# Kernel tuning notes

Measured on AMD Instinct MI355X. Metric: run time of the kernel, lower is better.

The kernel has to match this reference:

```python
import jax, jax.numpy as jnp
import numpy as np

B, T, K = 1024, 1024, 48
START, STOP = 46, 47
NEG = -10000.0


def setup_inputs() -> dict:
    key = jax.random.key(0)
    k1, k2 = jax.random.split(key)
    feats = jax.random.normal(k1, (B, T, K), dtype=jnp.float32)
    transitions = jax.random.normal(k2, (K, K), dtype=jnp.float32)
    # CRF constraints exactly as in __init__: no transition into START, none out of STOP
    transitions = transitions.at[START, :].set(NEG).at[:, STOP].set(NEG)
    return {"feats": feats, "transitions": transitions}


def _viterbi_one(feats, transitions):
    # feats: [T, K]; transitions[next_tag, prev_tag]: [K, K]
    init = jnp.full((K,), NEG, dtype=feats.dtype).at[START].set(0.0)

    def step(forward_var, feat):
        # scores[next, prev] = forward_var[prev] + transitions[next, prev]
        scores = forward_var[None, :] + transitions
        bptr = jnp.argmax(scores, axis=1)                 # [K] best prev per next
        new_fv = jnp.max(scores, axis=1) + feat           # [K]
        return new_fv, bptr

    forward_var, bptrs = jax.lax.scan(step, init, feats)  # bptrs: [T, K]
    terminal = forward_var + transitions[STOP]
    best = jnp.argmax(terminal)
    path_score = terminal[best]

    # backtrack: carry = tag at time t, emit it, move to bptrs[t][tag]
    def back(tag, bp):
        return bp[tag], tag

    _, best_path = jax.lax.scan(back, best, bptrs, reverse=True)  # [T] in time order
    return path_score, best_path


def reference(feats, transitions):
    # vmap the (faithful, per-sequence) Viterbi decode over the batch
    scores, paths = jax.vmap(_viterbi_one, in_axes=(0, None))(feats, transitions)
    return scores, paths
```

## Files before the change

### kernel.cpp

```cpp
#include <hip/hip_runtime.h>
#include <float.h>


#define BB 1024
#define TT 1024
#define KK 48
#define CC 16
#define LL 64
#define NEGV -10000.0f

__device__ __forceinline__ float rdlane(float v, int l) {
  return __int_as_float(__builtin_amdgcn_readlane(__float_as_int(v), l));
}
__device__ __forceinline__ float max3f(float a, float b, float c) {
  return fmaxf(fmaxf(a, b), c);
}


#define FSTEP(T_, FEAT_)                                                   \
  {                                                                        \
    float fvr[KK];                                                         \
    _Pragma("unroll") for (int j = 0; j < 12; ++j) {                       \
      float4 v4 = *(const float4*)(&fvbuf[4 * j]);                         \
      fvr[4 * j + 0] = v4.x; fvr[4 * j + 1] = v4.y;                        \
      fvr[4 * j + 2] = v4.z; fvr[4 * j + 3] = v4.w;                        \
    }                                                                      \
    float s_[KK];                                                          \
    _Pragma("unroll") for (int p = 0; p < KK; ++p) {                       \
      s_[p] = fvr[p] + tr[p];                                              \
    }                                                                      \
    float part[16];                                                        \
    _Pragma("unroll") for (int g = 0; g < 16; ++g) {                       \
      part[g] = max3f(s_[3 * g], s_[3 * g + 1], s_[3 * g + 2]);            \
    }                                                                      \
    float q0 = max3f(part[0], part[1], part[2]);                           \
    float q1 = max3f(part[3], part[4], part[5]);                           \
    float q2 = max3f(part[6], part[7], part[8]);                           \
    float q3 = max3f(part[9], part[10], part[11]);                         \
    float q4 = max3f(part[12], part[13], part[14]);                        \
    float m_ = fmaxf(max3f(q0, q1, q2), max3f(q3, q4, part[15]));          \
    mp[(size_t)(T_)*KK] = m_;                                              \
    fv = m_ + (FEAT_);                                                     \
    __builtin_amdgcn_wave_barrier();                                       \
    fvbuf[lane] = fv;                                                      \
    __builtin_amdgcn_wave_barrier();                                       \
  }

__global__ __launch_bounds__(64, 1) void viterbi_fused(
    const float* __restrict__ feats, const float* __restrict__ trans,
    float* __restrict__ scores, float* __restrict__ mx,
    float* __restrict__ path) {
  __shared__ __align__(16) float fvbuf[64];
  __shared__ float tl[KK * KK];
  const int lane = threadIdx.x;
  const int b = blockIdx.x;
  const int rl = (lane < KK) ? lane : (KK - 1);

  float tr[KK];
#pragma unroll
  for (int j = 0; j < 12; ++j) {
    float4 t4 = *(const float4*)(trans + rl * KK + 4 * j);
    tr[4 * j + 0] = t4.x; tr[4 * j + 1] = t4.y;
    tr[4 * j + 2] = t4.z; tr[4 * j + 3] = t4.w;
  }
#pragma unroll
  for (int j = 0; j < KK; ++j) asm volatile("" : "+v"(tr[j]));
  const float tstop = trans[(KK - 1) * KK + rl];
  for (int i = lane; i < KK * KK; i += 64) tl[i] = trans[i];

  const float* fp = feats + (size_t)b * TT * KK + rl;
  float* mp = mx + (size_t)b * TT * KK + rl;

  float fv = (lane == 46) ? 0.0f : NEGV;
  __syncthreads();
  fvbuf[lane] = fv;
  __builtin_amdgcn_wave_barrier();

  if (lane < KK) {
    float fA[8], fB[8];
#pragma unroll
    for (int k = 0; k < 8; ++k) fA[k] = fp[(size_t)k * KK];

    for (int t0 = 0; t0 < TT; t0 += 16) {
#pragma unroll
      for (int k = 0; k < 8; ++k)
        fB[k] = fp[(size_t)((t0 + 8 + k) & (TT - 1)) * KK];
#pragma unroll
      for (int u = 0; u < 8; ++u) FSTEP(t0 + u, fA[u]);
#pragma unroll
      for (int k = 0; k < 8; ++k)
        fA[k] = fp[(size_t)((t0 + 16 + k) & (TT - 1)) * KK];
#pragma unroll
      for (int u = 0; u < 8; ++u) FSTEP(t0 + 8 + u, fB[u]);
    }
  }

  float v = (lane < KK) ? (fv + tstop) : -FLT_MAX;
  int idx = lane;
#pragma unroll
  for (int off = 32; off >= 1; off >>= 1) {
    float ov = __shfl_xor(v, off);
    int oi = __shfl_xor(idx, off);
    bool take = (ov > v) || (ov == v && oi < idx);
    v = take ? ov : v;
    idx = take ? oi : idx;
  }
  if (lane == 0) scores[b] = v;
  int tag = idx;

  asm volatile("s_waitcnt vmcnt(0)" ::: "memory");

  float topA = mp[(size_t)(TT - 1) * KK];
  float MA[8], FE[8], MB[8], FB2[8];
#pragma unroll
  for (int u = 0; u < 8; ++u) {
    MA[u] = mp[(size_t)(TT - 2 - u) * KK];
    FE[u] = fp[(size_t)(TT - 2 - u) * KK];
  }

  int myv = 0;
  for (int jb = TT - 1; jb >= 15; jb -= 16) {
#pragma unroll
    for (int u = 0; u < 8; ++u) {
      int r = jb - 9 - u; int rc = r < 0 ? 0 : r;
      MB[u] = mp[(size_t)rc * KK];
      FB2[u] = fp[(size_t)rc * KK];
    }
#pragma unroll
    for (int u = 0; u < 8; ++u) {
      const int j = jb - u;
      if (lane == (j & 63)) myv = tag;
      if ((j & 63) == 0) path[(size_t)b * TT + j + lane] = (float)myv;
      float Tg = (u == 0) ? topA : MA[u - 1];
      float target = rdlane(Tg, tag);
      float s = (MA[u] + FE[u]) + tl[tag * KK + rl];
      unsigned long long bal = __ballot(s == target);
      tag = (int)__builtin_ctzll(bal);
    }
    float topB = MA[7];
#pragma unroll
    for (int u = 0; u < 8; ++u) {
      int r = jb - 17 - u; int rc = r < 0 ? 0 : r;
      MA[u] = mp[(size_t)rc * KK];
      FE[u] = fp[(size_t)rc * KK];
    }
#pragma unroll
    for (int u = 0; u < 8; ++u) {
      const int j = jb - 8 - u;
      if (lane == (j & 63)) myv = tag;
      if ((j & 63) == 0) path[(size_t)b * TT + j + lane] = (float)myv;
      float Tg = (u == 0) ? topB : MB[u - 1];
      float target = rdlane(Tg, tag);
      float s = (MB[u] + FB2[u]) + tl[tag * KK + rl];
      unsigned long long bal = __ballot(s == target);
      tag = (int)__builtin_ctzll(bal);
    }
    topA = MB[7];
  }
}


__global__ __launch_bounds__(64, 1) void viterbi_fwd_f(
    const float* __restrict__ feats, const float* __restrict__ trans,
    float* __restrict__ scores, unsigned char* __restrict__ bptr,
    int* __restrict__ bestArr) {
  __shared__ __align__(16) float fvbuf[64];
  const int lane = threadIdx.x;
  const int b = blockIdx.x;
  const int rl = (lane < KK) ? lane : (KK - 1);

  float tr[KK];
#pragma unroll
  for (int j = 0; j < 12; ++j) {
    float4 t4 = *(const float4*)(trans + rl * KK + 4 * j);
    tr[4 * j + 0] = t4.x; tr[4 * j + 1] = t4.y;
    tr[4 * j + 2] = t4.z; tr[4 * j + 3] = t4.w;
  }
  const float tstop = trans[(KK - 1) * KK + rl];

  if (lane < KK) fvbuf[lane] = (lane == 46) ? 0.0f : NEGV;
  __builtin_amdgcn_wave_barrier();

  const float* fp = feats + (size_t)b * TT * KK + rl;
  unsigned char* bp = bptr + (size_t)b * TT * KK + lane;

  float fbuf[4];
#pragma unroll
  for (int k = 0; k < 4; ++k) fbuf[k] = fp[(size_t)k * KK];

  float fv = NEGV;
  for (int t0 = 0; t0 < TT; t0 += 4) {
#pragma unroll
    for (int u = 0; u < 4; ++u) {
      const int t = t0 + u;
      float fvr[KK];
#pragma unroll
      for (int j = 0; j < 12; ++j) {
        float4 v4 = *(const float4*)(&fvbuf[4 * j]);
        fvr[4 * j + 0] = v4.x; fvr[4 * j + 1] = v4.y;
        fvr[4 * j + 2] = v4.z; fvr[4 * j + 3] = v4.w;
      }
      __builtin_amdgcn_wave_barrier();

      float bs0 = fvr[0] + tr[0], bs1 = fvr[12] + tr[12];
      float bs2 = fvr[24] + tr[24], bs3 = fvr[36] + tr[36];
      int bi0 = 0, bi1 = 12, bi2 = 24, bi3 = 36;
#pragma unroll
      for (int p = 1; p < 12; ++p) {
        float s0 = fvr[p] + tr[p];
        float s1 = fvr[12 + p] + tr[12 + p];
        float s2 = fvr[24 + p] + tr[24 + p];
        float s3 = fvr[36 + p] + tr[36 + p];
        if (s0 > bs0) { bs0 = s0; bi0 = p; }
        if (s1 > bs1) { bs1 = s1; bi1 = 12 + p; }
        if (s2 > bs2) { bs2 = s2; bi2 = 24 + p; }
        if (s3 > bs3) { bs3 = s3; bi3 = 36 + p; }
      }
      bool c1 = bs1 > bs0;
      float m01 = c1 ? bs1 : bs0; int i01 = c1 ? bi1 : bi0;
      bool c3 = bs3 > bs2;
      float m23 = c3 ? bs3 : bs2; int i23 = c3 ? bi3 : bi2;
      bool cf = m23 > m01;
      float m = cf ? m23 : m01; int bpi = cf ? i23 : i01;

      float nfv = m + fbuf[u];
      int tpre = t + 4; if (tpre >= TT) tpre = 0;
      fbuf[u] = fp[(size_t)tpre * KK];

      if (lane < KK) {
        bp[(size_t)t * KK] = (unsigned char)bpi;
        fvbuf[lane] = nfv;
        fv = nfv;
      }
      __builtin_amdgcn_wave_barrier();
    }
  }

  float v = (lane < KK) ? (fv + tstop) : -FLT_MAX;
  int idx = lane;
#pragma unroll
  for (int off = 32; off >= 1; off >>= 1) {
    float ov = __shfl_xor(v, off);
    int oi = __shfl_xor(idx, off);
    bool take = (ov > v) || (ov == v && oi < idx);
    v = take ? ov : v;
    idx = take ? oi : idx;
  }
  if (lane == 0) { scores[b] = v; bestArr[b] = idx; }
}

__global__ __launch_bounds__(256) void bwd_map(
    const unsigned char* __restrict__ bptr, unsigned char* __restrict__ cmap) {
  const int lane = threadIdx.x & 63;
  const int wg = blockIdx.x * 4 + (threadIdx.x >> 6);
  const int b = wg >> 4;
  const int c = wg & (CC - 1);
  const int rl = (lane < KK) ? lane : (KK - 1);
  const unsigned char* bp = bptr + ((size_t)b * TT + (size_t)c * LL) * KK + rl;

  int x = rl;
  const int CH = 16;
  int cur[CH], nxt[CH];
#pragma unroll
  for (int j = 0; j < CH; ++j) cur[j] = bp[(size_t)(LL - CH + j) * KK];
  for (int tb = LL - CH; tb >= 0; tb -= CH) {
    if (tb >= CH) {
#pragma unroll
      for (int j = 0; j < CH; ++j) nxt[j] = bp[(size_t)(tb - CH + j) * KK];
    }
#pragma unroll
    for (int j = CH - 1; j >= 0; --j) x = __shfl(cur[j], x);
    if (tb >= CH) {
#pragma unroll
      for (int j = 0; j < CH; ++j) cur[j] = nxt[j];
    }
  }
  if (lane < KK) cmap[(size_t)wg * KK + lane] = (unsigned char)x;
}

__global__ __launch_bounds__(256) void bwd_entry(
    const unsigned char* __restrict__ cmap, const int* __restrict__ bestArr,
    int* __restrict__ entry) {
  const int lane = threadIdx.x & 63;
  const int b = blockIdx.x * 4 + (threadIdx.x >> 6);
  const int rl = (lane < KK) ? lane : (KK - 1);

  int rows[CC];
#pragma unroll
  for (int c = 0; c < CC; ++c) rows[c] = cmap[((size_t)b * CC + c) * KK + rl];

  int tag = bestArr[b];
  int ev = 0;
#pragma unroll
  for (int c = CC - 1; c >= 0; --c) {
    if (lane == c) ev = tag;
    tag = __shfl(rows[c], tag);
  }
  if (lane < CC) entry[b * CC + lane] = ev;
}

__global__ __launch_bounds__(256) void bwd_emit(
    const unsigned char* __restrict__ bptr, const int* __restrict__ entry,
    float* __restrict__ path) {
  const int lane = threadIdx.x & 63;
  const int wg = blockIdx.x * 4 + (threadIdx.x >> 6);
  const int b = wg >> 4;
  const int c = wg & (CC - 1);
  const int rl = (lane < KK) ? lane : (KK - 1);
  const unsigned char* bp = bptr + ((size_t)b * TT + (size_t)c * LL) * KK + rl;

  int x = entry[b * CC + c];
  int myv = 0;
  const int CH = 16;
  int cur[CH], nxt[CH];
#pragma unroll
  for (int j = 0; j < CH; ++j) cur[j] = bp[(size_t)(LL - CH + j) * KK];
  for (int tb = LL - CH; tb >= 0; tb -= CH) {
    if (tb >= CH) {
#pragma unroll
      for (int j = 0; j < CH; ++j) nxt[j] = bp[(size_t)(tb - CH + j) * KK];
    }
#pragma unroll
    for (int j = CH - 1; j >= 0; --j) {
      if (lane == tb + j) myv = x;
      x = __shfl(cur[j], x);
    }
    if (tb >= CH) {
#pragma unroll
      for (int j = 0; j < CH; ++j) cur[j] = nxt[j];
    }
  }
  path[(size_t)b * TT + (size_t)c * LL + lane] = (float)myv;
}

extern "C" void kernel_launch(void* const* d_in, const int* in_sizes, int n_in,
                              void* d_out, int out_size, void* d_ws,
                              size_t ws_size, hipStream_t stream) {
  const float* feats = (const float*)d_in[0];
  const float* trans = (const float*)d_in[1];
  float* out = (float*)d_out;

  const size_t MX_BYTES = (size_t)BB * TT * KK * sizeof(float);
  if (ws_size >= MX_BYTES) {
    float* mx = (float*)d_ws;
    viterbi_fused<<<dim3(BB), dim3(64), 0, stream>>>(feats, trans, out, mx,
                                                     out + BB);
  } else {
    unsigned char* bptr = (unsigned char*)d_ws;
    char* p = (char*)d_ws + (size_t)BB * TT * KK;
    int* bestArr = (int*)p;
    p += BB * sizeof(int);
    unsigned char* cmap = (unsigned char*)p;
    p += (size_t)BB * CC * KK;
    int* entry = (int*)p;

    viterbi_fwd_f<<<dim3(BB), dim3(64), 0, stream>>>(feats, trans, out, bptr,
                                                     bestArr);
    bwd_map<<<dim3(BB * CC / 4), dim3(256), 0, stream>>>(bptr, cmap);
    bwd_entry<<<dim3(BB / 4), dim3(256), 0, stream>>>(cmap, bestArr, entry);
    bwd_emit<<<dim3(BB * CC / 4), dim3(256), 0, stream>>>(bptr, entry,
                                                          out + BB);
  }
}
```

Baseline: 481.9 us.

## Pack two sequences per block and interleave their backtracks in one wave

Each block now runs two waves, each doing the forward Viterbi pass for its own sequence. After a block barrier, the second wave exits and the first wave backtracks both sequences at once, interleaving their two dependent ballot/readlane chains. The aim is to hide the latency of the serial backtrack by giving each step two independent chains to overlap. In exchange, half the waves sit idle during the backtrack, the block is more coupled, and per-lane register use roughly doubles in that phase.

```diff
diff --git a/kernel.cpp b/kernel.cpp
--- a/kernel.cpp
+++ b/kernel.cpp
@@ -21,7 +21,7 @@
   {                                                                        \
     float fvr[KK];                                                         \
     _Pragma("unroll") for (int j = 0; j < 12; ++j) {                       \
-      float4 v4 = *(const float4*)(&fvbuf[4 * j]);                         \
+      float4 v4 = *(const float4*)(&fvb[4 * j]);                           \
       fvr[4 * j + 0] = v4.x; fvr[4 * j + 1] = v4.y;                        \
       fvr[4 * j + 2] = v4.z; fvr[4 * j + 3] = v4.w;                        \
     }                                                                      \
@@ -42,19 +42,24 @@
     mp[(size_t)(T_)*KK] = m_;                                              \
     fv = m_ + (FEAT_);                                                     \
     __builtin_amdgcn_wave_barrier();                                       \
-    fvbuf[lane] = fv;                                                      \
+    fvb[lane] = fv;                                                        \
     __builtin_amdgcn_wave_barrier();                                       \
   }
 
-__global__ __launch_bounds__(64, 1) void viterbi_fused(
+__global__ __launch_bounds__(128, 1) void viterbi_fused2(
     const float* __restrict__ feats, const float* __restrict__ trans,
     float* __restrict__ scores, float* __restrict__ mx,
     float* __restrict__ path) {
-  __shared__ __align__(16) float fvbuf[64];
+  __shared__ __align__(16) float fvbuf[2][64];
   __shared__ float tl[KK * KK];
-  const int lane = threadIdx.x;
-  const int b = blockIdx.x;
+  __shared__ int tagsh[2];
+  const int tid = threadIdx.x;
+  const int w = tid >> 6;
+  const int lane = tid & 63;
   const int rl = (lane < KK) ? lane : (KK - 1);
+  const int bA = blockIdx.x * 2;
+  const int b = bA + w;
+  float* fvb = &fvbuf[w][0];
 
   float tr[KK];
 #pragma unroll
@@ -66,14 +71,13 @@
 #pragma unroll
   for (int j = 0; j < KK; ++j) asm volatile("" : "+v"(tr[j]));
   const float tstop = trans[(KK - 1) * KK + rl];
-  for (int i = lane; i < KK * KK; i += 64) tl[i] = trans[i];
+  for (int i = tid; i < KK * KK; i += 128) tl[i] = trans[i];
 
   const float* fp = feats + (size_t)b * TT * KK + rl;
   float* mp = mx + (size_t)b * TT * KK + rl;
 
   float fv = (lane == 46) ? 0.0f : NEGV;
-  __syncthreads();
-  fvbuf[lane] = fv;
+  fvb[lane] = fv;
   __builtin_amdgcn_wave_barrier();
 
   if (lane < KK) {
@@ -105,57 +109,95 @@
     v = take ? ov : v;
     idx = take ? oi : idx;
   }
-  if (lane == 0) scores[b] = v;
-  int tag = idx;
-
-  asm volatile("s_waitcnt vmcnt(0)" ::: "memory");
-
-  float topA = mp[(size_t)(TT - 1) * KK];
-  float MA[8], FE[8], MB[8], FB2[8];
+  if (lane == 0) { scores[b] = v; tagsh[w] = idx; }
+
+  __syncthreads();
+  if (w == 1) return;
+
+  int tagA = tagsh[0], tagB = tagsh[1];
+  const float* fpA = fp;
+  const float* mpA = mp;
+  const float* fpB = feats + (size_t)(bA + 1) * TT * KK + rl;
+  const float* mpB = mx + (size_t)(bA + 1) * TT * KK + rl;
+  float* pathA = path + (size_t)bA * TT;
+  float* pathB = path + (size_t)(bA + 1) * TT;
+
+  float topA_A = mpA[(size_t)(TT - 1) * KK];
+  float topA_B = mpB[(size_t)(TT - 1) * KK];
+  float MAa[8], FEa[8], MBa[8], FBa[8];
+  float MAb[8], FEb[8], MBb[8], FBb[8];
 #pragma unroll
   for (int u = 0; u < 8; ++u) {
-    MA[u] = mp[(size_t)(TT - 2 - u) * KK];
-    FE[u] = fp[(size_t)(TT - 2 - u) * KK];
-  }
-
-  int myv = 0;
+    MAa[u] = mpA[(size_t)(TT - 2 - u) * KK];
+    FEa[u] = fpA[(size_t)(TT - 2 - u) * KK];
+    MAb[u] = mpB[(size_t)(TT - 2 - u) * KK];
+    FEb[u] = fpB[(size_t)(TT - 2 - u) * KK];
+  }
+
+  int myvA = 0, myvB = 0;
   for (int jb = TT - 1; jb >= 15; jb -= 16) {
 #pragma unroll
     for (int u = 0; u < 8; ++u) {
       int r = jb - 9 - u; int rc = r < 0 ? 0 : r;
-      MB[u] = mp[(size_t)rc * KK];
-      FB2[u] = fp[(size_t)rc * KK];
+      MBa[u] = mpA[(size_t)rc * KK];
+      FBa[u] = fpA[(size_t)rc * KK];
+      MBb[u] = mpB[(size_t)rc * KK];
+      FBb[u] = fpB[(size_t)rc * KK];
     }
 #pragma unroll
     for (int u = 0; u < 8; ++u) {
       const int j = jb - u;
-      if (lane == (j & 63)) myv = tag;
-      if ((j & 63) == 0) path[(size_t)b * TT + j + lane] = (float)myv;
-      float Tg = (u == 0) ? topA : MA[u - 1];
-      float target = rdlane(Tg, tag);
-      float s = (MA[u] + FE[u]) + tl[tag * KK + rl];
-      unsigned long long bal = __ballot(s == target);
-      tag = (int)__builtin_ctzll(bal);
-    }
-    float topB = MA[7];
+      if (lane == (j & 63)) { myvA = tagA; myvB = tagB; }
+      if ((j & 63) == 0) {
+        pathA[j + lane] = (float)myvA;
+        pathB[j + lane] = (float)myvB;
+      }
+      float tlA = tl[tagA * KK + rl];
+      float tlB = tl[tagB * KK + rl];
+      float TgA = (u == 0) ? topA_A : MAa[u - 1];
+      float TgB = (u == 0) ? topA_B : MAb[u - 1];
+      float tgtA = rdlane(TgA, tagA);
+      float tgtB = rdlane(TgB, tagB);
+      float sA = (MAa[u] + FEa[u]) + tlA;
+      float sB = (MAb[u] + FEb[u]) + tlB;
+      unsigned long long balA = __ballot(sA == tgtA);
+      unsigned long long balB = __ballot(sB == tgtB);
+      tagA = (int)__builtin_ctzll(balA);
+      tagB = (int)__builtin_ctzll(balB);
+    }
+    float topB_A = MAa[7];
+    float topB_B = MAb[7];
 #pragma unroll
     for (int u = 0; u < 8; ++u) {
       int r = jb - 17 - u; int rc = r < 0 ? 0 : r;
-      MA[u] = mp[(size_t)rc * KK];
-      FE[u] = fp[(size_t)rc * KK];
+      MAa[u] = mpA[(size_t)rc * KK];
+      FEa[u] = fpA[(size_t)rc * KK];
+      MAb[u] = mpB[(size_t)rc * KK];
+      FEb[u] = fpB[(size_t)rc * KK];
     }
 #pragma unroll
     for (int u = 0; u < 8; ++u) {
       const int j = jb - 8 - u;
-      if (lane == (j & 63)) myv = tag;
-      if ((j & 63) == 0) path[(size_t)b * TT + j + lane] = (float)myv;
-      float Tg = (u == 0) ? topB : MB[u - 1];
-      float target = rdlane(Tg, tag);
-      float s = (MB[u] + FB2[u]) + tl[tag * KK + rl];
-      unsigned long long bal = __ballot(s == target);
-      tag = (int)__builtin_ctzll(bal);
-    }
-    topA = MB[7];
+      if (lane == (j & 63)) { myvA = tagA; myvB = tagB; }
+      if ((j & 63) == 0) {
+        pathA[j + lane] = (float)myvA;
+        pathB[j + lane] = (float)myvB;
+      }
+      float tlA = tl[tagA * KK + rl];
+      float tlB = tl[tagB * KK + rl];
+      float TgA = (u == 0) ? topB_A : MBa[u - 1];
+      float TgB = (u == 0) ? topB_B : MBb[u - 1];
+      float tgtA = rdlane(TgA, tagA);
+      float tgtB = rdlane(TgB, tagB);
+      float sA = (MBa[u] + FBa[u]) + tlA;
+      float sB = (MBb[u] + FBb[u]) + tlB;
+      unsigned long long balA = __ballot(sA == tgtA);
+      unsigned long long balB = __ballot(sB == tgtB);
+      tagA = (int)__builtin_ctzll(balA);
+      tagB = (int)__builtin_ctzll(balB);
+    }
+    topA_A = MBa[7];
+    topA_B = MBb[7];
   }
 }
 
@@ -343,8 +385,8 @@
   const size_t MX_BYTES = (size_t)BB * TT * KK * sizeof(float);
   if (ws_size >= MX_BYTES) {
     float* mx = (float*)d_ws;
-    viterbi_fused<<<dim3(BB), dim3(64), 0, stream>>>(feats, trans, out, mx,
-                                                     out + BB);
+    viterbi_fused2<<<dim3(BB / 2), dim3(128), 0, stream>>>(feats, trans, out,
+                                                           mx, out + BB);
   } else {
     unsigned char* bptr = (unsigned char*)d_ws;
     char* p = (char*)d_ws + (size_t)BB * TT * KK;
```

Result: slower. 513.8 us (+6.6%).
